# Kernel tuning notes

Hardware: AMD Instinct MI355X
Metric: run time of the kernel (lower is better)

Reference implementation:

```python
import jax, jax.numpy as jnp
import numpy as np

N_EMBD = 1024
N_EXPERTS = 8
TOP_K = 2
D_FF = 4 * N_EMBD


def setup_inputs() -> dict:
    key = jax.random.key(0)
    ks = jax.random.split(key, 7)
    s_in = 1.0 / np.sqrt(N_EMBD)
    s_ff = 1.0 / np.sqrt(D_FF)
    return {
        "x": jax.random.normal(ks[0], (2, 2048, N_EMBD), dtype=jnp.float32),
        "Wr": jax.random.normal(ks[1], (N_EMBD, N_EXPERTS), dtype=jnp.float32) * s_in,
        "br": jnp.zeros((N_EXPERTS,), dtype=jnp.float32),
        "W1": jax.random.normal(ks[2], (N_EXPERTS, N_EMBD, D_FF), dtype=jnp.float32) * s_in,
        "b1": jnp.zeros((N_EXPERTS, D_FF), dtype=jnp.float32),
        "W2": jax.random.normal(ks[3], (N_EXPERTS, D_FF, N_EMBD), dtype=jnp.float32) * s_ff,
        "b2": jnp.zeros((N_EXPERTS, N_EMBD), dtype=jnp.float32),
    }


def _moe_forward(x, Wr, br, W1, b1, W2, b2):
    b, t, e = x.shape
    flat_x = x.reshape(-1, e)                      # [T, d]
    T = flat_x.shape[0]
    # --- TopKRouter: logits -> top_k -> sparse softmax over selected experts ---
    logits = flat_x @ Wr + br                      # [T, E]
    top_vals, top_idx = jax.lax.top_k(logits, TOP_K)
    neg_inf = jnp.full_like(logits, -jnp.inf)
    masked = neg_inf.at[jnp.arange(T)[:, None], top_idx].set(top_vals)
    probs = jax.nn.softmax(masked, axis=-1)        # [T, E], zeros outside top-k
    # --- Per-expert FFN, weighted combine (dense weights make this a sum) ---
    out = jnp.zeros_like(flat_x)
    for ei in range(N_EXPERTS):
        h = jax.nn.relu(flat_x @ W1[ei] + b1[ei])  # [T, 4d]
        y = h @ W2[ei] + b2[ei]                    # [T, d]
        out = out + probs[:, ei:ei + 1] * y
    return out.reshape(b, t, e)


def reference(x, Wr, br, W1, b1, W2, b2):
    return _moe_forward(x, Wr, br, W1, b1, W2, b2)
```

## Files before the change

### kernel.cpp

```cpp
#include <hip/hip_runtime.h>
#include <cstdio>
#include <cstdint>

#define TOKS 4096
#define DMODEL 1024
#define DFF 4096
#define NEXP 8

typedef __bf16 bf16_8 __attribute__((ext_vector_type(8)));
typedef float f32x4 __attribute__((ext_vector_type(4)));
typedef __attribute__((address_space(1))) const void* gptr_t;
typedef __attribute__((address_space(3))) void* lptr_t;

__device__ __forceinline__ unsigned short f2bf(float f) {
  unsigned int u = __builtin_bit_cast(unsigned int, f);
  u += 0x7FFFu + ((u >> 16) & 1u);
  return (unsigned short)(u >> 16);
}

__global__ __launch_bounds__(256) void transpose_cast_k(const float* __restrict__ in,
                                                        unsigned short* __restrict__ out,
                                                        int R, int C) {
  __shared__ float tile[64][65];
  const float* inm = in + (size_t)blockIdx.y * R * C;
  unsigned short* outm = out + (size_t)blockIdx.y * R * C;
  int tcn = C >> 6;
  int tr = blockIdx.x / tcn, tc = blockIdx.x % tcn;
  int r0 = tr << 6, c0 = tc << 6;
  int tid = threadIdx.x;
  int lr = tid >> 6, lc = tid & 63;
#pragma unroll
  for (int i = 0; i < 16; ++i)
    tile[lr + 4 * i][lc] = inm[(size_t)(r0 + lr + 4 * i) * C + c0 + lc];
  __syncthreads();
#pragma unroll
  for (int i = 0; i < 8; ++i) {
    int row = (tid >> 5) + i * 8;
    int colu = tid & 31;
    float f0 = tile[colu * 2][row];
    float f1 = tile[colu * 2 + 1][row];
    unsigned int u = (unsigned int)f2bf(f0) | ((unsigned int)f2bf(f1) << 16);
    *(unsigned int*)(outm + (size_t)(c0 + row) * R + r0 + colu * 2) = u;
  }
}

__global__ __launch_bounds__(256) void cast_x_k(const float* __restrict__ x,
                                                unsigned short* __restrict__ xb) {
  int i = blockIdx.x * 256 + threadIdx.x;
  float4 f = ((const float4*)x)[i];
  ushort4 u;
  u.x = f2bf(f.x); u.y = f2bf(f.y); u.z = f2bf(f.z); u.w = f2bf(f.w);
  ((ushort4*)xb)[i] = u;
}

__global__ __launch_bounds__(256) void router_k(const float* __restrict__ x,
                                                const float* __restrict__ Wr,
                                                const float* __restrict__ br,
                                                int* __restrict__ cnt,
                                                int* __restrict__ list,
                                                float* __restrict__ plist) {
  int t = blockIdx.x * 4 + (threadIdx.x >> 6);
  int lane = threadIdx.x & 63;
  float a[NEXP];
#pragma unroll
  for (int e = 0; e < NEXP; ++e) a[e] = 0.f;
  const float* xr = x + (size_t)t * DMODEL;
  for (int i = lane; i < DMODEL; i += 64) {
    float xv = xr[i];
    const float* wr = Wr + (size_t)i * NEXP;
#pragma unroll
    for (int e = 0; e < NEXP; ++e) a[e] += xv * wr[e];
  }
#pragma unroll
  for (int off = 32; off > 0; off >>= 1) {
#pragma unroll
    for (int e = 0; e < NEXP; ++e) a[e] += __shfl_xor(a[e], off);
  }
  if (lane == 0) {
#pragma unroll
    for (int e = 0; e < NEXP; ++e) a[e] += br[e];
    int i0 = 0; float m0 = a[0];
#pragma unroll
    for (int e = 1; e < NEXP; ++e) if (a[e] > m0) { m0 = a[e]; i0 = e; }
    int i1 = -1; float m1 = -1e30f;
#pragma unroll
    for (int e = 0; e < NEXP; ++e) if (e != i0 && a[e] > m1) { m1 = a[e]; i1 = e; }
    float tt = expf(m1 - m0);
    float p0 = 1.f / (1.f + tt);
    float p1 = 1.f - p0;
    int pos0 = atomicAdd(&cnt[i0], 1);
    list[i0 * TOKS + pos0] = t; plist[i0 * TOKS + pos0] = p0;
    int pos1 = atomicAdd(&cnt[i1], 1);
    list[i1 * TOKS + pos1] = t; plist[i1 * TOKS + pos1] = p1;
  }
}

__global__ void offsets_k(const int* __restrict__ cnt, int* __restrict__ off) {
  if (threadIdx.x == 0) {
    int s = 0;
    for (int e = 0; e < NEXP; ++e) { off[e] = s; s += cnt[e]; }
    off[NEXP] = s;
  }
}

template <int MODE>
__global__ __launch_bounds__(256) void moe_gemm_k(
    const unsigned short* __restrict__ Abase, const unsigned short* __restrict__ Bbase,
    const float* __restrict__ bias, const int* __restrict__ cnt, const int* __restrict__ off,
    const int* __restrict__ list, const float* __restrict__ plist,
    unsigned short* __restrict__ Hout, float* __restrict__ Out) {
  constexpr int K = (MODE == 0) ? DMODEL : DFF;
  constexpr int NN = (MODE == 0) ? DFF : DMODEL;
  const int e = blockIdx.z;
  const int ce = cnt[e];
  const int m0 = blockIdx.y * 128;
  if (m0 >= ce) return;
  const int rem = ce - m0;
  const int n0 = blockIdx.x * 128;
  const int oe = off[e];

  __shared__ unsigned short As[8192];
  __shared__ unsigned short Bs[8192];

  const int tid = threadIdx.x;
  const int lane = tid & 63;
  const int w = tid >> 6;
  const int wm = w >> 1, wn = w & 1;

  const unsigned short* Bm = Bbase + (size_t)e * NN * K;
  const int g = (tid & 7) ^ ((tid >> 3) & 7);

  size_t a_src[4], b_src[4];
#pragma unroll
  for (int c = 0; c < 4; ++c) {
    int row = c * 32 + (tid >> 3);
    int rr = row < rem ? row : 0;
    size_t arow;
    if (MODE == 0) arow = (size_t)list[e * TOKS + m0 + rr];
    else           arow = (size_t)(oe + m0 + rr);
    a_src[c] = arow * K + g * 8;
    b_src[c] = (size_t)(n0 + row) * K + g * 8;
  }

  f32x4 acc[4][4];
#pragma unroll
  for (int i = 0; i < 4; ++i)
#pragma unroll
    for (int j = 0; j < 4; ++j) acc[i][j] = (f32x4){0.f, 0.f, 0.f, 0.f};

  for (int k0 = 0; k0 < K; k0 += 64) {
    __syncthreads();
#pragma unroll
    for (int c = 0; c < 4; ++c) {
      __builtin_amdgcn_global_load_lds((gptr_t)(Abase + a_src[c] + k0),
                                       (lptr_t)&As[(c * 256 + w * 64) * 8], 16, 0, 0);
      __builtin_amdgcn_global_load_lds((gptr_t)(Bm + b_src[c] + k0),
                                       (lptr_t)&Bs[(c * 256 + w * 64) * 8], 16, 0, 0);
    }
    __syncthreads();
#pragma unroll
    for (int kk = 0; kk < 2; ++kk) {
      bf16_8 av[4], bv[4];
#pragma unroll
      for (int fr = 0; fr < 4; ++fr) {
        int row = wm * 64 + fr * 16 + (lane & 15);
        int slot = row * 8 + ((kk * 4 + (lane >> 4)) ^ (row & 7));
        av[fr] = *(const bf16_8*)&As[slot * 8];
      }
#pragma unroll
      for (int fc = 0; fc < 4; ++fc) {
        int row = wn * 64 + fc * 16 + (lane & 15);
        int slot = row * 8 + ((kk * 4 + (lane >> 4)) ^ (row & 7));
        bv[fc] = *(const bf16_8*)&Bs[slot * 8];
      }
#pragma unroll
      for (int fr = 0; fr < 4; ++fr)
#pragma unroll
        for (int fc = 0; fc < 4; ++fc)
          acc[fr][fc] = __builtin_amdgcn_mfma_f32_16x16x32_bf16(av[fr], bv[fc],
                                                                acc[fr][fc], 0, 0, 0);
    }
  }

  if (MODE == 0) {
    const float* be = bias + (size_t)e * NN + n0;
#pragma unroll
    for (int fr = 0; fr < 4; ++fr) {
#pragma unroll
      for (int j = 0; j < 4; ++j) {
        int row = wm * 64 + fr * 16 + (lane >> 4) * 4 + j;
        if (row < rem) {
          unsigned short* hr = Hout + (size_t)(oe + m0 + row) * DFF + n0;
#pragma unroll
          for (int fc = 0; fc < 4; ++fc) {
            int col = wn * 64 + fc * 16 + (lane & 15);
            float v = acc[fr][fc][j] + be[col];
            hr[col] = f2bf(fmaxf(v, 0.f));
          }
        }
      }
    }
  } else {
    const float* be = bias + (size_t)e * NN + n0;
#pragma unroll
    for (int fr = 0; fr < 4; ++fr) {
#pragma unroll
      for (int j = 0; j < 4; ++j) {
        int row = wm * 64 + fr * 16 + (lane >> 4) * 4 + j;
        if (row < rem) {
          int tok = list[e * TOKS + m0 + row];
          float p = plist[e * TOKS + m0 + row];
          float* orow = Out + (size_t)tok * DMODEL + n0;
#pragma unroll
          for (int fc = 0; fc < 4; ++fc) {
            int col = wn * 64 + fc * 16 + (lane & 15);
            atomicAdd(&orow[col], p * (acc[fr][fc][j] + be[col]));
          }
        }
      }
    }
  }
}

extern "C" void kernel_launch(void* const* d_in, const int* in_sizes, int n_in,
                              void* d_out, int out_size, void* d_ws, size_t ws_size,
                              hipStream_t stream) {
  const float* x  = (const float*)d_in[0];
  const float* Wr = (const float*)d_in[1];
  const float* br = (const float*)d_in[2];
  const float* W1 = (const float*)d_in[3];
  const float* b1 = (const float*)d_in[4];
  const float* W2 = (const float*)d_in[5];
  const float* b2 = (const float*)d_in[6];
  float* out = (float*)d_out;

  const size_t SZ_W = (size_t)NEXP * DMODEL * DFF;
  char* ws = (char*)d_ws;
  size_t o = 0;
  unsigned short* W1t = (unsigned short*)(ws + o); o += SZ_W * 2;
  unsigned short* W2t = (unsigned short*)(ws + o); o += SZ_W * 2;
  unsigned short* xb  = (unsigned short*)(ws + o); o += (size_t)TOKS * DMODEL * 2;
  unsigned short* h   = (unsigned short*)(ws + o); o += (size_t)2 * TOKS * DFF * 2;
  int*   cnt   = (int*)(ws + o);   o += 256;
  int*   offp  = (int*)(ws + o);   o += 256;
  int*   list  = (int*)(ws + o);   o += (size_t)NEXP * TOKS * 4;
  float* plist = (float*)(ws + o); o += (size_t)NEXP * TOKS * 4;
  if (o > ws_size) {
    fprintf(stderr, "kernel_launch: ws too small: need %zu have %zu\n", o, ws_size);
    hipMemsetAsync(d_out, 0, (size_t)out_size * 4, stream);
    return;
  }

  hipMemsetAsync(cnt, 0, 256, stream);
  hipMemsetAsync(d_out, 0, (size_t)out_size * 4, stream);

  transpose_cast_k<<<dim3((DMODEL / 64) * (DFF / 64), NEXP), 256, 0, stream>>>(W1, W1t, DMODEL, DFF);
  transpose_cast_k<<<dim3((DFF / 64) * (DMODEL / 64), NEXP), 256, 0, stream>>>(W2, W2t, DFF, DMODEL);
  cast_x_k<<<TOKS * DMODEL / 4 / 256, 256, 0, stream>>>(x, xb);
  router_k<<<TOKS / 4, 256, 0, stream>>>(x, Wr, br, cnt, list, plist);
  offsets_k<<<1, 64, 0, stream>>>(cnt, offp);
  moe_gemm_k<0><<<dim3(DFF / 128, TOKS / 128, NEXP), 256, 0, stream>>>(
      xb, W1t, b1, cnt, offp, list, plist, h, nullptr);
  moe_gemm_k<1><<<dim3(DMODEL / 128, TOKS / 128, NEXP), 256, 0, stream>>>(
      h, W2t, b2, cnt, offp, list, plist, nullptr, out);
}
```

Baseline: 767.6 us.

## Double-buffer LDS tiles and remap workgroups for XCD-local locality

Splits the K loop into stage and compute phases with two LDS buffers, so global-to-LDS loads for the next tile overlap MFMA work on the current one. This halves the barriers per step. Workgroup indices are also permuted so that consecutive tiles of an expert land on the same XCD, to improve L2 reuse of weights. LDS usage doubles, which may lower occupancy.

Result: faster. 750.7 us (-2.2%).

```diff
diff --git a/kernel.cpp b/kernel.cpp
--- a/kernel.cpp
+++ b/kernel.cpp
@@ -111,16 +111,25 @@
     unsigned short* __restrict__ Hout, float* __restrict__ Out) {
   constexpr int K = (MODE == 0) ? DMODEL : DFF;
   constexpr int NN = (MODE == 0) ? DFF : DMODEL;
-  const int e = blockIdx.z;
+  constexpr int NT = NN / 128;
+  constexpr int NWG = NEXP * 32 * NT;
+  constexpr int CHUNK = NWG / 8;
+
+  const int flat = blockIdx.x + NT * (blockIdx.y + 32 * blockIdx.z);
+  const int u = (flat & 7) * CHUNK + (flat >> 3);
+  const int nt = u % NT;
+  const int mt = (u / NT) & 31;
+  const int e = u / (NT * 32);
+
   const int ce = cnt[e];
-  const int m0 = blockIdx.y * 128;
+  const int m0 = mt * 128;
   if (m0 >= ce) return;
   const int rem = ce - m0;
-  const int n0 = blockIdx.x * 128;
+  const int n0 = nt * 128;
   const int oe = off[e];
 
-  __shared__ unsigned short As[8192];
-  __shared__ unsigned short Bs[8192];
+  __shared__ unsigned short As[2][8192];
+  __shared__ unsigned short Bs[2][8192];
 
   const int tid = threadIdx.x;
   const int lane = tid & 63;
@@ -148,16 +157,17 @@
 #pragma unroll
     for (int j = 0; j < 4; ++j) acc[i][j] = (f32x4){0.f, 0.f, 0.f, 0.f};
 
-  for (int k0 = 0; k0 < K; k0 += 64) {
-    __syncthreads();
+  auto STAGE = [&](int buf, int k0) {
 #pragma unroll
     for (int c = 0; c < 4; ++c) {
       __builtin_amdgcn_global_load_lds((gptr_t)(Abase + a_src[c] + k0),
-                                       (lptr_t)&As[(c * 256 + w * 64) * 8], 16, 0, 0);
+                                       (lptr_t)&As[buf][(c * 256 + w * 64) * 8], 16, 0, 0);
       __builtin_amdgcn_global_load_lds((gptr_t)(Bm + b_src[c] + k0),
-                                       (lptr_t)&Bs[(c * 256 + w * 64) * 8], 16, 0, 0);
-    }
-    __syncthreads();
+                                       (lptr_t)&Bs[buf][(c * 256 + w * 64) * 8], 16, 0, 0);
+    }
+  };
+
+  auto COMPUTE = [&](int buf) {
 #pragma unroll
     for (int kk = 0; kk < 2; ++kk) {
       bf16_8 av[4], bv[4];
@@ -165,13 +175,13 @@
       for (int fr = 0; fr < 4; ++fr) {
         int row = wm * 64 + fr * 16 + (lane & 15);
         int slot = row * 8 + ((kk * 4 + (lane >> 4)) ^ (row & 7));
-        av[fr] = *(const bf16_8*)&As[slot * 8];
+        av[fr] = *(const bf16_8*)&As[buf][slot * 8];
       }
 #pragma unroll
       for (int fc = 0; fc < 4; ++fc) {
         int row = wn * 64 + fc * 16 + (lane & 15);
         int slot = row * 8 + ((kk * 4 + (lane >> 4)) ^ (row & 7));
-        bv[fc] = *(const bf16_8*)&Bs[slot * 8];
+        bv[fc] = *(const bf16_8*)&Bs[buf][slot * 8];
       }
 #pragma unroll
       for (int fr = 0; fr < 4; ++fr)
@@ -180,7 +190,19 @@
           acc[fr][fc] = __builtin_amdgcn_mfma_f32_16x16x32_bf16(av[fr], bv[fc],
                                                                 acc[fr][fc], 0, 0, 0);
     }
-  }
+  };
+
+  constexpr int NSTEP = K / 64;
+  STAGE(0, 0);
+  __syncthreads();
+  int cur = 0;
+  for (int t = 0; t < NSTEP - 1; ++t) {
+    STAGE(cur ^ 1, (t + 1) * 64);
+    COMPUTE(cur);
+    __syncthreads();
+    cur ^= 1;
+  }
+  COMPUTE(cur);
 
   if (MODE == 0) {
     const float* be = bias + (size_t)e * NN + n0;
```
